# Kernel optimization log

Measured on AMD Instinct MI355X. Metric: run time of the kernel, lower is better.

Reference implementation:

```python
import jax, jax.numpy as jnp
import numpy as np

DIM = 1024
HEADS = 16
DIM_HEAD = 64
INNER = HEADS * DIM_HEAD  # == DIM, so project_out Linear is shape-consistent
SCALE = DIM_HEAD ** -0.5
EPS = 1e-5


def setup_inputs() -> dict:
    key = jax.random.key(0)
    ks = jax.random.split(key, 8)
    std = 0.02
    return {
        "x": jax.random.normal(ks[0], (2, 2048, DIM), dtype=jnp.float32),
        "gamma": jnp.ones((DIM,), dtype=jnp.float32),
        "beta": jnp.zeros((DIM,), dtype=jnp.float32),
        "wq": jax.random.normal(ks[1], (DIM, INNER), dtype=jnp.float32) * std,
        "wk": jax.random.normal(ks[2], (DIM, INNER), dtype=jnp.float32) * std,
        "wv": jax.random.normal(ks[3], (DIM, INNER), dtype=jnp.float32) * std,
        "wo": jax.random.normal(ks[4], (INNER, DIM), dtype=jnp.float32) * std,
        "w_out": jax.random.normal(ks[5], (INNER, DIM), dtype=jnp.float32) * std,
        "b_out": jnp.zeros((DIM,), dtype=jnp.float32),
    }


def reference(x, gamma, beta, wq, wk, wv, wo, w_out, b_out):
    b, n, d = x.shape
    # LayerNorm
    mu = jnp.mean(x, axis=-1, keepdims=True)
    var = jnp.mean(jnp.square(x - mu), axis=-1, keepdims=True)
    xn = (x - mu) * jax.lax.rsqrt(var + EPS) * gamma + beta
    # QKV projections -> [b, h, n, dh]
    def split_heads(t):
        return t.reshape(b, n, HEADS, DIM_HEAD).transpose(0, 2, 1, 3)
    q = split_heads(xn @ wq)
    k = split_heads(xn @ wk)
    v = split_heads(xn @ wv)
    scores = jnp.einsum('bhqd,bhkd->bhqk', q, k) * SCALE
    attn = jax.nn.softmax(scores, axis=-1)
    out = jnp.einsum('bhqk,bhkd->bhqd', attn, v)
    out = out.transpose(0, 2, 1, 3).reshape(b, n, INNER)
    out = out @ wo               # wo: inner -> dim
    out = out @ w_out + b_out    # project_out Linear (dropout=0 -> identity)
    return out
```

## Files before the change

### kernel.cpp

```cpp
#include <hip/hip_runtime.h>

typedef _Float16 f16;
typedef _Float16 f16x2 __attribute__((ext_vector_type(2)));
typedef _Float16 f16x4 __attribute__((ext_vector_type(4)));
typedef _Float16 f16x8 __attribute__((ext_vector_type(8)));
typedef float f32x4 __attribute__((ext_vector_type(4)));
typedef float f32x16 __attribute__((ext_vector_type(16)));

#define MFMA_F16(a, b, c) __builtin_amdgcn_mfma_f32_16x16x32_f16(a, b, c, 0, 0, 0)
#define MFMA32_F16(a, b, c) __builtin_amdgcn_mfma_f32_32x32x16_f16(a, b, c, 0, 0, 0)
#define ASYNC16(g, l) __builtin_amdgcn_global_load_lds(                              \
    (const __attribute__((address_space(1))) void*)(g),                              \
    (__attribute__((address_space(3))) void*)(l), 16, 0, 0)

__global__ __launch_bounds__(256)
void pre_kernel(const float* __restrict__ x, const float* __restrict__ gamma,
                const float* __restrict__ beta, f16* __restrict__ xn,
                const float* __restrict__ wq, const float* __restrict__ wk,
                const float* __restrict__ wv, const float* __restrict__ wo,
                const float* __restrict__ wout,
                f16* __restrict__ wqt, f16* __restrict__ wkt, f16* __restrict__ wvt,
                f16* __restrict__ wo_h, f16* __restrict__ woutt)
{
    const int t = threadIdx.x;
    if (blockIdx.x < 4096) {
        const int row = blockIdx.x;
        const float* xr = x + (size_t)row * 1024;
        float4 v = *(const float4*)(xr + t * 4);
        float s  = v.x + v.y + v.z + v.w;
        float ss = v.x * v.x + v.y * v.y + v.z * v.z + v.w * v.w;
#pragma unroll
        for (int off = 32; off > 0; off >>= 1) {
            s  += __shfl_down(s, off);
            ss += __shfl_down(ss, off);
        }
        __shared__ float wsum[4], wsq[4];
        const int wid = t >> 6, lane = t & 63;
        if (lane == 0) { wsum[wid] = s; wsq[wid] = ss; }
        __syncthreads();
        const float fs  = wsum[0] + wsum[1] + wsum[2] + wsum[3];
        const float fss = wsq[0] + wsq[1] + wsq[2] + wsq[3];
        const float mu  = fs * (1.0f / 1024.0f);
        const float var = fss * (1.0f / 1024.0f) - mu * mu;
        const float rs  = rsqrtf(var + 1e-5f);
        float4 g = *(const float4*)(gamma + t * 4);
        float4 b = *(const float4*)(beta + t * 4);
        f16x4 o;
        o[0] = (f16)((v.x - mu) * rs * g.x + b.x);
        o[1] = (f16)((v.y - mu) * rs * g.y + b.y);
        o[2] = (f16)((v.z - mu) * rs * g.z + b.z);
        o[3] = (f16)((v.w - mu) * rs * g.w + b.w);
        *(f16x4*)(xn + (size_t)row * 1024 + t * 4) = o;
        return;
    }
    const int pb = blockIdx.x - 4096;
    const int z = pb >> 8, rem = pb & 255;
    const int bx = rem & 15, by = rem >> 4;
    const float* src; f16* dst; int tr; float scl = 1.0f;
    switch (z) {
        case 0:  src = wq;   dst = wqt;   tr = 1; scl = 0.18033688011f; break;
        case 1:  src = wk;   dst = wkt;   tr = 1; break;
        case 2:  src = wv;   dst = wvt;   tr = 1; break;
        case 3:  src = wo;   dst = wo_h;  tr = 0; break;
        default: src = wout; dst = woutt; tr = 1; break;
    }
    const int r0 = by * 64, c0 = bx * 64;
    if (!tr) {
#pragma unroll
        for (int i = 0; i < 16; i++) {
            int idx = t + 256 * i;
            int r = idx >> 6, c = idx & 63;
            dst[(size_t)(r0 + r) * 1024 + c0 + c] = (f16)src[(size_t)(r0 + r) * 1024 + c0 + c];
        }
    } else {
        __shared__ __align__(16) f16 T[64][72];
#pragma unroll
        for (int i = 0; i < 16; i++) {
            int idx = t + 256 * i;
            int r = idx >> 6, c = idx & 63;
            T[r][c] = (f16)(src[(size_t)(r0 + r) * 1024 + c0 + c] * scl);
        }
        __syncthreads();
#pragma unroll
        for (int i = 0; i < 16; i++) {
            int idx = t + 256 * i;
            int r = idx >> 6, c = idx & 63;
            dst[(size_t)(c0 + r) * 1024 + r0 + c] = T[c][r];
        }
    }
}

__global__ __launch_bounds__(256, 3)
void gemm_qkv_w2(const f16* __restrict__ A, const f16* __restrict__ Bt,
                 f16* __restrict__ Qd, f16* __restrict__ Kd, f16* __restrict__ Vd,
                 const f16* __restrict__ A2, const f16* __restrict__ Bt2,
                 f16* __restrict__ W2t)
{
    __shared__ __align__(16) f16 smem[2 * 128 * 64];
    f16* As = smem;
    f16* Bs = smem + 128 * 64;
    const int tid = threadIdx.x;
    const int wid = tid >> 6, lane = tid & 63;
    const int qq = lane >> 4, ml = lane & 15;
    const int row0 = (wid >> 1) * 64, col0 = (wid & 1) * 64;

    int mode, bx, by;
    const f16 *Abase, *Bbase;
    if (blockIdx.y < 24) {
        mode = 0; bx = blockIdx.x; by = blockIdx.y; Abase = A; Bbase = Bt;
    } else {
        mode = 1;
        int id = (blockIdx.y - 24) * 32 + blockIdx.x;
        bx = id & 7; by = id >> 3; Abase = A2; Bbase = Bt2;
    }
    const f16* Ab = Abase + (size_t)bx * 128 * 1024;
    const f16* Bb = Bbase + (size_t)by * 128 * 1024;
    const int sr = lane >> 3;
    const int sc = ((lane & 7) ^ sr) * 8;
    const int swz = ml & 7;

    f32x4 acc[4][4];
#pragma unroll
    for (int i = 0; i < 4; i++)
#pragma unroll
        for (int j = 0; j < 4; j++) acc[i][j] = (f32x4){0.f, 0.f, 0.f, 0.f};

    for (int k0 = 0; k0 < 1024; k0 += 64) {
        __syncthreads();
#pragma unroll
        for (int j = 0; j < 4; j++) {
            const int inst = wid * 4 + j;
            const int r = inst * 8 + sr;
            ASYNC16(Ab + (size_t)r * 1024 + k0 + sc, &As[inst * 512]);
            ASYNC16(Bb + (size_t)r * 1024 + k0 + sc, &Bs[inst * 512]);
        }
        __syncthreads();
#pragma unroll
        for (int kh = 0; kh < 2; kh++) {
            f16x8 af[4], bf[4];
#pragma unroll
            for (int mb = 0; mb < 4; mb++)
                af[mb] = *(const f16x8*)(&As[(row0 + mb * 16 + ml) * 64 + ((kh * 4 + qq) ^ swz) * 8]);
#pragma unroll
            for (int nb = 0; nb < 4; nb++)
                bf[nb] = *(const f16x8*)(&Bs[(col0 + nb * 16 + ml) * 64 + ((kh * 4 + qq) ^ swz) * 8]);
#pragma unroll
            for (int mb = 0; mb < 4; mb++)
#pragma unroll
                for (int nb = 0; nb < 4; nb++)
                    acc[mb][nb] = MFMA_F16(af[mb], bf[nb], acc[mb][nb]);
        }
    }

    if (mode == 1) {
        const int rT = bx * 128 + row0 + qq * 4;
#pragma unroll
        for (int mb = 0; mb < 4; mb++)
#pragma unroll
            for (int nb = 0; nb < 4; nb++) {
                int c = by * 128 + col0 + nb * 16 + ml;
#pragma unroll
                for (int rg = 0; rg < 4; rg++)
                    W2t[(size_t)(rT + mb * 16 + rg) * 1024 + c] = (f16)acc[mb][nb][rg];
            }
        return;
    }
    __syncthreads();
    f16* Cs = smem;
    const int sel = (by * 128) >> 10;
    const int bb  = (bx * 128) >> 11;
    const int nl0 = (bx * 128) & 2047;
    const int h0  = (by & 7) * 2;
    if (sel < 2) {
#pragma unroll
        for (int mb = 0; mb < 4; mb++)
#pragma unroll
            for (int nb = 0; nb < 4; nb++) {
                int col = col0 + nb * 16 + ml;
#pragma unroll
                for (int rg = 0; rg < 4; rg++) {
                    int row = row0 + mb * 16 + qq * 4 + rg;
                    int ch = (col >> 3) ^ (row & 15);
                    Cs[row * 128 + ch * 8 + (col & 7)] = (f16)acc[mb][nb][rg];
                }
            }
        __syncthreads();
        f16* Dst = (sel == 0 ? Qd : Kd);
#pragma unroll
        for (int i = 0; i < 8; i++) {
            int idx = i * 256 + tid;
            int r = idx >> 4, ch = idx & 15;
            f16x8 v = *(const f16x8*)(&Cs[r * 128 + ((ch ^ (r & 15)) * 8)]);
            int hh = h0 + (ch >> 3), d0 = (ch & 7) * 8;
            *(f16x8*)(Dst + ((size_t)(bb * 16 + hh) * 2048 + nl0 + r) * 64 + d0) = v;
        }
    } else {
#pragma unroll
        for (int mb = 0; mb < 4; mb++)
#pragma unroll
            for (int nb = 0; nb < 4; nb++) {
                int col = col0 + nb * 16 + ml;
                int rch = ((row0 + mb * 16) >> 3) + (qq >> 1);
                int ch = rch ^ (col & 15);
                f16x4 w;
                w[0] = (f16)acc[mb][nb][0]; w[1] = (f16)acc[mb][nb][1];
                w[2] = (f16)acc[mb][nb][2]; w[3] = (f16)acc[mb][nb][3];
                *(f16x4*)(&Cs[col * 128 + ch * 8 + (qq & 1) * 4]) = w;
            }
        __syncthreads();
#pragma unroll
        for (int i = 0; i < 8; i++) {
            int idx = i * 256 + tid;
            int c = idx >> 4, tc = idx & 15;
            f16x8 v = *(const f16x8*)(&Cs[c * 128 + ((tc ^ (c & 15)) * 8)]);
            int hh = h0 + (c >> 6), d = c & 63;
            *(f16x8*)(Vd + ((size_t)(bb * 16 + hh) * 64 + d) * 2048 + nl0 + tc * 8) = v;
        }
    }
}

__global__ __launch_bounds__(128, 4)
void flash_kernel(const f16* __restrict__ Q, const f16* __restrict__ K,
                  const f16* __restrict__ Vt, f16* __restrict__ O)
{
    __shared__ __align__(16) f16 Ks[2][64 * 64];
    __shared__ __align__(16) f16 Vts[2][64 * 64];

    const int bh = blockIdx.y;
    const int q0 = blockIdx.x * 64;
    const int tid = threadIdx.x, wid = tid >> 6, lane = tid & 63;
    const int ql = lane & 31;
    const int h  = lane >> 5;
    const int sw = ql & 7;

    const f16* Qb = Q + ((size_t)bh * 2048 + q0 + wid * 32) * 64;
    const f16* Kb = K + (size_t)bh * 2048 * 64;
    const f16* Vb = Vt + (size_t)bh * 64 * 2048;

    f16x8 qf[4];
#pragma unroll
    for (int kt = 0; kt < 4; kt++)
        qf[kt] = *(const f16x8*)(Qb + (size_t)ql * 64 + kt * 16 + h * 8);

    f32x16 oacc[2];
#pragma unroll
    for (int db = 0; db < 2; db++)
#pragma unroll
        for (int r = 0; r < 16; r++) oacc[db][r] = 0.f;
    float lsum = 0.f;

    const int sr = lane >> 3, scw = ((lane & 7) ^ sr) * 8;

#pragma unroll
    for (int j = 0; j < 4; j++) {
        const int inst = wid * 4 + j;
        const int r = inst * 8 + sr;
        ASYNC16(Kb + (size_t)r * 64 + scw, &Ks[0][inst * 512]);
        ASYNC16(Vb + (size_t)r * 2048 + scw, &Vts[0][inst * 512]);
    }
    __syncthreads();

    for (int t = 0; t < 32; t++) {
        const int buf = t & 1;
        if (t < 31) {
            const int t1 = (t + 1) * 64;
#pragma unroll
            for (int j = 0; j < 4; j++) {
                const int inst = wid * 4 + j;
                const int r = inst * 8 + sr;
                ASYNC16(Kb + ((size_t)t1 + r) * 64 + scw, &Ks[buf ^ 1][inst * 512]);
                ASYNC16(Vb + (size_t)r * 2048 + t1 + scw, &Vts[buf ^ 1][inst * 512]);
            }
        }

        f32x16 s0, s1;
#pragma unroll
        for (int r = 0; r < 16; r++) { s0[r] = 0.f; s1[r] = 0.f; }
#pragma unroll
        for (int kt = 0; kt < 4; kt++) {
            const int ch = ((kt * 2 + h) ^ sw) * 8;
            f16x8 kf0 = *(const f16x8*)(&Ks[buf][ql * 64 + ch]);
            f16x8 kf1 = *(const f16x8*)(&Ks[buf][(32 + ql) * 64 + ch]);
            s0 = MFMA32_F16(kf0, qf[kt], s0);
            s1 = MFMA32_F16(kf1, qf[kt], s1);
        }

        f16x2 pk[2][8], xp[2][8];
#pragma unroll
        for (int i = 0; i < 8; i++) {
            float a0 = __builtin_amdgcn_exp2f(s0[2 * i]);
            float a1 = __builtin_amdgcn_exp2f(s0[2 * i + 1]);
            float b0 = __builtin_amdgcn_exp2f(s1[2 * i]);
            float b1 = __builtin_amdgcn_exp2f(s1[2 * i + 1]);
            lsum += (a0 + a1) + (b0 + b1);
            pk[0][i] = __builtin_bit_cast(f16x2, __builtin_amdgcn_cvt_pkrtz(a0, a1));
            pk[1][i] = __builtin_bit_cast(f16x2, __builtin_amdgcn_cvt_pkrtz(b0, b1));
        }
#pragma unroll
        for (int kb = 0; kb < 2; kb++)
#pragma unroll
            for (int i = 0; i < 8; i++)
                xp[kb][i] = __builtin_bit_cast(f16x2,
                    __shfl_xor(__builtin_bit_cast(int, pk[kb][i]), 32));

#pragma unroll
        for (int kt = 0; kt < 4; kt++) {
            const int kb = kt >> 1, c = (kt & 1) * 4;
            f16x2 b0 = h ? xp[kb][c + 2] : pk[kb][c];
            f16x2 b1 = h ? xp[kb][c + 3] : pk[kb][c + 1];
            f16x2 b2 = h ? pk[kb][c + 2] : xp[kb][c];
            f16x2 b3 = h ? pk[kb][c + 3] : xp[kb][c + 1];
            f16x8 pb;
            pb[0] = b0[0]; pb[1] = b0[1]; pb[2] = b1[0]; pb[3] = b1[1];
            pb[4] = b2[0]; pb[5] = b2[1]; pb[6] = b3[0]; pb[7] = b3[1];
            const int ch = ((kt * 2 + h) ^ sw) * 8;
            f16x8 vf0 = *(const f16x8*)(&Vts[buf][ql * 64 + ch]);
            f16x8 vf1 = *(const f16x8*)(&Vts[buf][(32 + ql) * 64 + ch]);
            oacc[0] = MFMA32_F16(vf0, pb, oacc[0]);
            oacc[1] = MFMA32_F16(vf1, pb, oacc[1]);
        }
        __syncthreads();
    }

    lsum += __builtin_bit_cast(float, __shfl_xor(__builtin_bit_cast(int, lsum), 32));
    const float linv = 1.0f / lsum;

    const int bb = bh >> 4, hh = bh & 15;
    const int tok = q0 + wid * 32 + ql;
    f16* Ob = O + ((size_t)(bb * 2048 + tok)) * 1024 + hh * 64 + 4 * h;
#pragma unroll
    for (int db = 0; db < 2; db++)
#pragma unroll
        for (int m = 0; m < 4; m++) {
            f16x2 lo = __builtin_bit_cast(f16x2, __builtin_amdgcn_cvt_pkrtz(
                oacc[db][4 * m] * linv, oacc[db][4 * m + 1] * linv));
            f16x2 hi = __builtin_bit_cast(f16x2, __builtin_amdgcn_cvt_pkrtz(
                oacc[db][4 * m + 2] * linv, oacc[db][4 * m + 3] * linv));
            f16x4 w; w[0] = lo[0]; w[1] = lo[1]; w[2] = hi[0]; w[3] = hi[1];
            *(f16x4*)(Ob + db * 32 + m * 8) = w;
        }
}

__global__ __launch_bounds__(256, 4)
void gemm_final(const f16* __restrict__ A, const f16* __restrict__ Bt,
                float* __restrict__ C, const float* __restrict__ bias)
{
    __shared__ __align__(16) f16 As[64 * 64];
    __shared__ __align__(16) f16 Bs[64 * 64];
    const int tid = threadIdx.x;
    const int wid = tid >> 6, lane = tid & 63;
    const int qq = lane >> 4, ml = lane & 15;
    const int row0 = (wid >> 1) * 32, col0 = (wid & 1) * 32;
    const f16* Ab = A + (size_t)blockIdx.x * 64 * 1024;
    const f16* Bb = Bt + (size_t)blockIdx.y * 64 * 1024;
    const int sr = lane >> 3;
    const int sc = ((lane & 7) ^ sr) * 8;
    const int swz = ml & 7;

    f32x4 acc[2][2];
#pragma unroll
    for (int i = 0; i < 2; i++)
#pragma unroll
        for (int j = 0; j < 2; j++) acc[i][j] = (f32x4){0.f, 0.f, 0.f, 0.f};

    for (int k0 = 0; k0 < 1024; k0 += 64) {
        __syncthreads();
#pragma unroll
        for (int j = 0; j < 2; j++) {
            const int inst = wid * 2 + j;
            const int r = inst * 8 + sr;
            ASYNC16(Ab + (size_t)r * 1024 + k0 + sc, &As[inst * 512]);
            ASYNC16(Bb + (size_t)r * 1024 + k0 + sc, &Bs[inst * 512]);
        }
        __syncthreads();
#pragma unroll
        for (int kh = 0; kh < 2; kh++) {
            f16x8 af[2], bf[2];
#pragma unroll
            for (int mb = 0; mb < 2; mb++)
                af[mb] = *(const f16x8*)(&As[(row0 + mb * 16 + ml) * 64 + ((kh * 4 + qq) ^ swz) * 8]);
#pragma unroll
            for (int nb = 0; nb < 2; nb++)
                bf[nb] = *(const f16x8*)(&Bs[(col0 + nb * 16 + ml) * 64 + ((kh * 4 + qq) ^ swz) * 8]);
#pragma unroll
            for (int mb = 0; mb < 2; mb++)
#pragma unroll
                for (int nb = 0; nb < 2; nb++)
                    acc[mb][nb] = MFMA_F16(af[mb], bf[nb], acc[mb][nb]);
        }
    }

    const int rT = blockIdx.x * 64 + row0 + qq * 4;
#pragma unroll
    for (int mb = 0; mb < 2; mb++)
#pragma unroll
        for (int nb = 0; nb < 2; nb++) {
            int c = blockIdx.y * 64 + col0 + nb * 16 + ml;
            float bv = bias[c];
#pragma unroll
            for (int rg = 0; rg < 4; rg++)
                C[(size_t)(rT + mb * 16 + rg) * 1024 + c] = acc[mb][nb][rg] + bv;
        }
}

extern "C" void kernel_launch(void* const* d_in, const int* in_sizes, int n_in,
                              void* d_out, int out_size, void* d_ws, size_t ws_size,
                              hipStream_t stream)
{
    const float* x     = (const float*)d_in[0];
    const float* gamma = (const float*)d_in[1];
    const float* beta  = (const float*)d_in[2];
    const float* wq    = (const float*)d_in[3];
    const float* wk    = (const float*)d_in[4];
    const float* wv    = (const float*)d_in[5];
    const float* wo    = (const float*)d_in[6];
    const float* wout  = (const float*)d_in[7];
    const float* bout  = (const float*)d_in[8];
    float* out = (float*)d_out;

    char* ws = (char*)d_ws;
    const size_t MB = 1 << 20;
    f16* xn    = (f16*)(ws + 0);
    f16* wqt   = (f16*)(ws + 8 * MB);
    f16* wkt   = (f16*)(ws + 10 * MB);
    f16* wvt   = (f16*)(ws + 12 * MB);
    f16* wo_h  = (f16*)(ws + 14 * MB);
    f16* woutt = (f16*)(ws + 16 * MB);
    f16* W2t   = (f16*)(ws + 18 * MB);
    f16* Qh    = (f16*)(ws + 20 * MB);
    f16* Kh    = (f16*)(ws + 28 * MB);
    f16* Vth   = (f16*)(ws + 36 * MB);
    f16* Oh    = xn;

    pre_kernel<<<5376, 256, 0, stream>>>(x, gamma, beta, xn, wq, wk, wv, wo, wout,
                                         wqt, wkt, wvt, wo_h, woutt);
    gemm_qkv_w2<<<dim3(32, 26), 256, 0, stream>>>(xn, wqt, Qh, Kh, Vth,
                                                  woutt, wo_h, W2t);
    flash_kernel<<<dim3(32, 32), 128, 0, stream>>>(Qh, Kh, Vth, Oh);
    gemm_final<<<dim3(64, 16), 256, 0, stream>>>(Oh, W2t, out, bout);
}
```

Before: 216.9 us.

## Split flash attention KV range in two and merge partials in final GEMM

The flash kernel now processes 128 queries per 256-thread block and splits the key/value sequence into two halves via blockIdx.z. Each half writes an unnormalized fp16 partial output and its row sums. The final GEMM loads both partials, adds them, scales by the reciprocal of the combined row sum per head, and then runs the MFMAs. This doubles the number of active waves in attention to improve occupancy and latency hiding. The cost is an extra partial-output buffer read in the GEMM, extra elementwise work in its inner loop, and a risk of fp16 range or precision loss from storing unnormalized accumulators.

```diff
diff --git a/kernel.cpp b/kernel.cpp
--- a/kernel.cpp
+++ b/kernel.cpp
@@ -219,23 +219,25 @@
     }
 }
 
-__global__ __launch_bounds__(128, 4)
+__global__ __launch_bounds__(256, 2)
 void flash_kernel(const f16* __restrict__ Q, const f16* __restrict__ K,
-                  const f16* __restrict__ Vt, f16* __restrict__ O)
+                  const f16* __restrict__ Vt, f16* __restrict__ Op0,
+                  f16* __restrict__ Op1, float* __restrict__ lp)
 {
     __shared__ __align__(16) f16 Ks[2][64 * 64];
     __shared__ __align__(16) f16 Vts[2][64 * 64];
 
     const int bh = blockIdx.y;
-    const int q0 = blockIdx.x * 64;
+    const int q0 = blockIdx.x * 128;
+    const int ks = blockIdx.z;
     const int tid = threadIdx.x, wid = tid >> 6, lane = tid & 63;
     const int ql = lane & 31;
     const int h  = lane >> 5;
     const int sw = ql & 7;
 
     const f16* Qb = Q + ((size_t)bh * 2048 + q0 + wid * 32) * 64;
-    const f16* Kb = K + (size_t)bh * 2048 * 64;
-    const f16* Vb = Vt + (size_t)bh * 64 * 2048;
+    const f16* Kb = K + (size_t)bh * 2048 * 64 + (size_t)ks * 1024 * 64;
+    const f16* Vb = Vt + (size_t)bh * 64 * 2048 + ks * 1024;
 
     f16x8 qf[4];
 #pragma unroll
@@ -252,21 +254,21 @@
     const int sr = lane >> 3, scw = ((lane & 7) ^ sr) * 8;
 
 #pragma unroll
-    for (int j = 0; j < 4; j++) {
-        const int inst = wid * 4 + j;
+    for (int j = 0; j < 2; j++) {
+        const int inst = wid * 2 + j;
         const int r = inst * 8 + sr;
         ASYNC16(Kb + (size_t)r * 64 + scw, &Ks[0][inst * 512]);
         ASYNC16(Vb + (size_t)r * 2048 + scw, &Vts[0][inst * 512]);
     }
     __syncthreads();
 
-    for (int t = 0; t < 32; t++) {
+    for (int t = 0; t < 16; t++) {
         const int buf = t & 1;
-        if (t < 31) {
+        if (t < 15) {
             const int t1 = (t + 1) * 64;
 #pragma unroll
-            for (int j = 0; j < 4; j++) {
-                const int inst = wid * 4 + j;
+            for (int j = 0; j < 2; j++) {
+                const int inst = wid * 2 + j;
                 const int r = inst * 8 + sr;
                 ASYNC16(Kb + ((size_t)t1 + r) * 64 + scw, &Ks[buf ^ 1][inst * 512]);
                 ASYNC16(Vb + (size_t)r * 2048 + t1 + scw, &Vts[buf ^ 1][inst * 512]);
@@ -323,40 +325,59 @@
     }
 
     lsum += __builtin_bit_cast(float, __shfl_xor(__builtin_bit_cast(int, lsum), 32));
-    const float linv = 1.0f / lsum;
 
     const int bb = bh >> 4, hh = bh & 15;
     const int tok = q0 + wid * 32 + ql;
-    f16* Ob = O + ((size_t)(bb * 2048 + tok)) * 1024 + hh * 64 + 4 * h;
+    if (h == 0) lp[(size_t)ks * 65536 + bh * 2048 + tok] = lsum;
+
+    f16* Op = ks ? Op1 : Op0;
+    f16* Ob = Op + ((size_t)(bb * 2048 + tok)) * 1024 + hh * 64 + 4 * h;
 #pragma unroll
     for (int db = 0; db < 2; db++)
 #pragma unroll
         for (int m = 0; m < 4; m++) {
             f16x2 lo = __builtin_bit_cast(f16x2, __builtin_amdgcn_cvt_pkrtz(
-                oacc[db][4 * m] * linv, oacc[db][4 * m + 1] * linv));
+                oacc[db][4 * m], oacc[db][4 * m + 1]));
             f16x2 hi = __builtin_bit_cast(f16x2, __builtin_amdgcn_cvt_pkrtz(
-                oacc[db][4 * m + 2] * linv, oacc[db][4 * m + 3] * linv));
+                oacc[db][4 * m + 2], oacc[db][4 * m + 3]));
             f16x4 w; w[0] = lo[0]; w[1] = lo[1]; w[2] = hi[0]; w[3] = hi[1];
             *(f16x4*)(Ob + db * 32 + m * 8) = w;
         }
 }
 
 __global__ __launch_bounds__(256, 4)
-void gemm_final(const f16* __restrict__ A, const f16* __restrict__ Bt,
+void gemm_final(const f16* __restrict__ A0, const f16* __restrict__ A1,
+                const f16* __restrict__ Bt, const float* __restrict__ lp,
                 float* __restrict__ C, const float* __restrict__ bias)
 {
-    __shared__ __align__(16) f16 As[64 * 64];
+    __shared__ __align__(16) f16 As0[64 * 64];
+    __shared__ __align__(16) f16 As1[64 * 64];
     __shared__ __align__(16) f16 Bs[64 * 64];
+    __shared__ f16 lh[16][64];
     const int tid = threadIdx.x;
     const int wid = tid >> 6, lane = tid & 63;
     const int qq = lane >> 4, ml = lane & 15;
     const int row0 = (wid >> 1) * 32, col0 = (wid & 1) * 32;
-    const f16* Ab = A + (size_t)blockIdx.x * 64 * 1024;
+    const int r0g = blockIdx.x * 64;
+    const f16* Ab0 = A0 + (size_t)r0g * 1024;
+    const f16* Ab1 = A1 + (size_t)r0g * 1024;
     const f16* Bb = Bt + (size_t)blockIdx.y * 64 * 1024;
     const int sr = lane >> 3;
     const int sc = ((lane & 7) ^ sr) * 8;
     const int swz = ml & 7;
 
+    {
+        const int bb = r0g >> 11, t0 = r0g & 2047;
+#pragma unroll
+        for (int i = 0; i < 4; i++) {
+            int idx = tid * 4 + i;
+            int hh = idx >> 6, r = idx & 63;
+            size_t li = (size_t)(bb * 16 + hh) * 2048 + t0 + r;
+            float l = lp[li] + lp[65536 + li];
+            lh[hh][r] = (f16)(1.0f / l);
+        }
+    }
+
     f32x4 acc[2][2];
 #pragma unroll
     for (int i = 0; i < 2; i++)
@@ -369,16 +390,29 @@
         for (int j = 0; j < 2; j++) {
             const int inst = wid * 2 + j;
             const int r = inst * 8 + sr;
-            ASYNC16(Ab + (size_t)r * 1024 + k0 + sc, &As[inst * 512]);
+            ASYNC16(Ab0 + (size_t)r * 1024 + k0 + sc, &As0[inst * 512]);
+            ASYNC16(Ab1 + (size_t)r * 1024 + k0 + sc, &As1[inst * 512]);
             ASYNC16(Bb + (size_t)r * 1024 + k0 + sc, &Bs[inst * 512]);
         }
         __syncthreads();
+        const int hd = k0 >> 6;
+        f16 scl[2];
+#pragma unroll
+        for (int mb = 0; mb < 2; mb++) scl[mb] = lh[hd][row0 + mb * 16 + ml];
 #pragma unroll
         for (int kh = 0; kh < 2; kh++) {
             f16x8 af[2], bf[2];
 #pragma unroll
-            for (int mb = 0; mb < 2; mb++)
-                af[mb] = *(const f16x8*)(&As[(row0 + mb * 16 + ml) * 64 + ((kh * 4 + qq) ^ swz) * 8]);
+            for (int mb = 0; mb < 2; mb++) {
+                const int off = (row0 + mb * 16 + ml) * 64 + ((kh * 4 + qq) ^ swz) * 8;
+                f16x8 a0 = *(const f16x8*)(&As0[off]);
+                f16x8 a1 = *(const f16x8*)(&As1[off]);
+                f16x8 sum = a0 + a1;
+                f16x8 av;
+#pragma unroll
+                for (int e = 0; e < 8; e++) av[e] = sum[e] * scl[mb];
+                af[mb] = av;
+            }
 #pragma unroll
             for (int nb = 0; nb < 2; nb++)
                 bf[nb] = *(const f16x8*)(&Bs[(col0 + nb * 16 + ml) * 64 + ((kh * 4 + qq) ^ swz) * 8]);
@@ -390,7 +424,7 @@
         }
     }
 
-    const int rT = blockIdx.x * 64 + row0 + qq * 4;
+    const int rT = r0g + row0 + qq * 4;
 #pragma unroll
     for (int mb = 0; mb < 2; mb++)
 #pragma unroll
@@ -430,12 +464,14 @@
     f16* Qh    = (f16*)(ws + 20 * MB);
     f16* Kh    = (f16*)(ws + 28 * MB);
     f16* Vth   = (f16*)(ws + 36 * MB);
-    f16* Oh    = xn;
+    f16* Op0   = xn;
+    f16* Op1   = (f16*)(ws + 8 * MB);
+    float* lp  = (float*)(ws + 16 * MB);
 
     pre_kernel<<<5376, 256, 0, stream>>>(x, gamma, beta, xn, wq, wk, wv, wo, wout,
                                          wqt, wkt, wvt, wo_h, woutt);
     gemm_qkv_w2<<<dim3(32, 26), 256, 0, stream>>>(xn, wqt, Qh, Kh, Vth,
                                                   woutt, wo_h, W2t);
-    flash_kernel<<<dim3(32, 32), 128, 0, stream>>>(Qh, Kh, Vth, Oh);
-    gemm_final<<<dim3(64, 16), 256, 0, stream>>>(Oh, W2t, out, bout);
+    flash_kernel<<<dim3(16, 32, 2), 256, 0, stream>>>(Qh, Kh, Vth, Op0, Op1, lp);
+    gemm_final<<<dim3(64, 16), 256, 0, stream>>>(Op0, Op1, W2t, lp, out, bout);
 }
```

After: 207.2 us. 1.05x faster.
